# Kernel tuning notes

Measured on AMD Instinct MI355X. Metric: run time of the kernel, lower is better.

## Reference

```python
import jax, jax.numpy as jnp
import numpy as np

B, N, IN_DIM, OUT_DIM, H = 8, 1024, 256, 256, 4
HD = OUT_DIM // H  # head_dim = 64
NEG = -1e9
EPS = 1e-5


def setup_inputs() -> dict:
    key = jax.random.key(0)
    ks = jax.random.split(key, 9)
    h = jax.random.normal(ks[0], (B, N, IN_DIM), dtype=jnp.float32)
    adj = jax.random.randint(ks[1], (N, N), 0, 2, dtype=jnp.int32)
    adj = adj.at[jnp.arange(N), jnp.arange(N)].set(1)  # self loops so no empty rows
    s = 1.0 / np.sqrt(IN_DIM)
    W = jax.random.uniform(ks[2], (H, IN_DIM, HD), jnp.float32, -s, s)
    sa = 1.0 / np.sqrt(2 * HD)
    a1 = jax.random.uniform(ks[3], (H, HD), jnp.float32, -sa, sa)
    a2 = jax.random.uniform(ks[4], (H, HD), jnp.float32, -sa, sa)
    sp = 1.0 / np.sqrt(OUT_DIM)
    proj_w = jax.random.uniform(ks[5], (OUT_DIM, OUT_DIM), jnp.float32, -sp, sp)
    proj_b = jax.random.uniform(ks[6], (OUT_DIM,), jnp.float32, -sp, sp)
    gamma = jnp.ones((OUT_DIM,), jnp.float32)
    beta = jnp.zeros((OUT_DIM,), jnp.float32)
    return {"h": h, "adj": adj, "W": W, "a1": a1, "a2": a2,
            "proj_w": proj_w, "proj_b": proj_b, "gamma": gamma, "beta": beta}


def reference(h, adj, W, a1, a2, proj_w, proj_b, gamma, beta):
    # Wh: [B,H,N,HD]
    Wh = jnp.einsum('bni,hid->bhnd', h, W)
    # Decompose a([Wh_i || Wh_j]) = a1.Wh_i + a2.Wh_j (same math as concat+linear)
    si = jnp.einsum('bhnd,hd->bhn', Wh, a1)  # [B,H,N]
    sj = jnp.einsum('bhnd,hd->bhn', Wh, a2)
    e = jax.nn.leaky_relu(si[:, :, :, None] + sj[:, :, None, :], 0.2)  # [B,H,N,N]
    mask = (adj == 0)  # [N,N]
    e = jnp.where(mask[None, None], NEG, e)
    alpha = jax.nn.softmax(e, axis=-1)
    out = jnp.einsum('bhnm,bhmd->bhnd', alpha, Wh)  # [B,H,N,HD]
    h_multi = out.transpose(0, 2, 1, 3).reshape(B, N, OUT_DIM)  # concat heads
    h_out = jnp.einsum('bnd,od->bno', h_multi, proj_w) + proj_b
    h_out = h_out + h  # residual (in_dim == out_dim)
    mu = jnp.mean(h_out, axis=-1, keepdims=True)
    var = jnp.mean(jnp.square(h_out - mu), axis=-1, keepdims=True)
    return (h_out - mu) * jax.lax.rsqrt(var + EPS) * gamma + beta
```

## Files before the change

kernel.cpp:

```cpp
#include <hip/hip_runtime.h>
#include <hip/hip_bf16.h>

#define NN 1024
#define LOG2E 1.44269504088896f

typedef __attribute__((ext_vector_type(8))) short short8;
typedef __attribute__((ext_vector_type(4))) short short4e;
typedef __attribute__((ext_vector_type(4))) float floatx4;
typedef __attribute__((ext_vector_type(4))) int intx4;
typedef __attribute__((ext_vector_type(2))) int intx2;

static __device__ __forceinline__ unsigned pk2(float f0, float f1) {
    unsigned u0 = __float_as_uint(f0) + 0x8000u;
    unsigned u1 = __float_as_uint(f1) + 0x8000u;
    return __builtin_amdgcn_perm(u1, u0, 0x07060302u);
}
static __device__ __forceinline__ short8 pk8(floatx4 v0, floatx4 v1) {
    union { intx4 i; short8 s; } u;
    u.i[0] = (int)pk2(v0[0], v0[1]); u.i[1] = (int)pk2(v0[2], v0[3]);
    u.i[2] = (int)pk2(v1[0], v1[1]); u.i[3] = (int)pk2(v1[2], v1[3]);
    return u.s;
}

__global__ __launch_bounds__(256) void prep_kernel(
    const float* __restrict__ W, const float* __restrict__ proj_w,
    const int* __restrict__ adj,
    __hip_bfloat16* __restrict__ WTb,
    __hip_bfloat16* __restrict__ pwb,
    unsigned* __restrict__ adjm)
{
    int blk = blockIdx.x, t = threadIdx.x;
    if (blk < 16) {
        int o = blk * 16 + (t >> 4);
        int hh = o >> 6, d = o & 63;
        #pragma unroll
        for (int kk = 0; kk < 16; ++kk) {
            int k = (t & 15) + 16 * kk;
            WTb[(size_t)o * 256 + k] = __float2bfloat16(W[((size_t)hh * 256 + k) * 64 + d]);
        }
    } else if (blk < 32) {
        size_t base = (size_t)(blk - 16) * 4096 + (size_t)t * 16;
        #pragma unroll
        for (int k = 0; k < 16; k += 8) {
            floatx4 v0 = *(const floatx4*)(proj_w + base + k);
            floatx4 v1 = *(const floatx4*)(proj_w + base + k + 4);
            *(short8*)(pwb + base + k) = pk8(v0, v1);
        }
    } else {
        int n = (blk - 32) * 8 + (t >> 5);
        int wd = t & 31;
        const int* arow = adj + (size_t)n * NN + wd * 32;
        unsigned bits = 0;
        #pragma unroll
        for (int j4 = 0; j4 < 8; ++j4) {
            intx4 v = *(const intx4*)(arow + j4 * 4);
            #pragma unroll
            for (int j = 0; j < 4; ++j) if (v[j] != 0) bits |= (1u << (j4 * 4 + j));
        }
        adjm[(size_t)n * 32 + wd] = bits;
    }
}

__global__ __launch_bounds__(256) void wh_kernel(
    const float* __restrict__ h,
    const __hip_bfloat16* __restrict__ WTb,
    const float* __restrict__ a1, const float* __restrict__ a2,
    __hip_bfloat16* __restrict__ WhT,
    float* __restrict__ si, float* __restrict__ sj)
{
    int t = threadIdx.x;
    int w = t >> 6, l = t & 63;
    int rl = l & 15, q = l >> 4;
    int r0 = blockIdx.x * 16;
    int bb = r0 >> 10, n0 = r0 & 1023;

    __shared__ __align__(16) __hip_bfloat16 bst[4][16][264];
    __shared__ float redsi[4][4][16];
    __shared__ float redsj[4][4][16];

    short8 af[8];
    const float* Arow = h + (size_t)(r0 + rl) * 256 + q * 8;
    #pragma unroll
    for (int k0 = 0; k0 < 8; ++k0) {
        floatx4 v0 = *(const floatx4*)(Arow + k0 * 32);
        floatx4 v1 = *(const floatx4*)(Arow + k0 * 32 + 4);
        af[k0] = pk8(v0, v1);
    }

    short8 sreg[8], nreg[8];
    {
        const __hip_bfloat16* src = WTb + (size_t)w * 16 * 256;
        #pragma unroll
        for (int k = 0; k < 8; ++k) sreg[k] = *(const short8*)(src + k * 512 + l * 8);
    }

    #pragma unroll
    for (int j = 0; j < 4; ++j) {
        if (j < 3) {
            const __hip_bfloat16* src = WTb + (size_t)(w + 4 * (j + 1)) * 16 * 256;
            #pragma unroll
            for (int k = 0; k < 8; ++k) nreg[k] = *(const short8*)(src + k * 512 + l * 8);
        }
        #pragma unroll
        for (int k = 0; k < 8; ++k)
            *(short8*)(&bst[w][k * 2 + (l >> 5)][(l & 31) * 8]) = sreg[k];
        floatx4 acc = {0.f, 0.f, 0.f, 0.f};
        #pragma unroll
        for (int k0 = 0; k0 < 8; ++k0) {
            short8 bf = *(const short8*)(&bst[w][rl][q * 8 + k0 * 32]);
            acc = __builtin_amdgcn_mfma_f32_16x16x32_bf16(af[k0], bf, acc, 0, 0, 0);
        }

        intx2 pr;
        pr[0] = (int)pk2(acc[0], acc[1]);
        pr[1] = (int)pk2(acc[2], acc[3]);
        *(intx2*)(WhT + ((size_t)(bb * 4 + j) * 64 + w * 16 + rl) * NN + n0 + q * 4) = pr;

        float av1 = a1[j * 64 + w * 16 + rl] * LOG2E;
        float av2 = a2[j * 64 + w * 16 + rl] * LOG2E;
        #pragma unroll
        for (int i = 0; i < 4; ++i) {
            float p1 = acc[i] * av1, p2 = acc[i] * av2;
            #pragma unroll
            for (int off = 1; off < 16; off <<= 1) {
                p1 += __shfl_xor(p1, off, 64);
                p2 += __shfl_xor(p2, off, 64);
            }
            if (rl == 0) { redsi[w][j][q * 4 + i] = p1; redsj[w][j][q * 4 + i] = p2; }
        }
        #pragma unroll
        for (int z = 0; z < 8; ++z) sreg[z] = nreg[z];
    }
    __syncthreads();

    if (t < 64) {
        int head = t >> 4, row = t & 15;
        si[(size_t)(bb * 4 + head) * NN + n0 + row] =
            redsi[0][head][row] + redsi[1][head][row] + redsi[2][head][row] + redsi[3][head][row];
    } else if (t < 128) {
        int u = t - 64;
        int head = u >> 4, row = u & 15;
        sj[(size_t)(bb * 4 + head) * NN + n0 + row] =
            redsj[0][head][row] + redsj[1][head][row] + redsj[2][head][row] + redsj[3][head][row];
    }
}

__global__ __launch_bounds__(256) void attn_kernel(
    const unsigned* __restrict__ adjm,
    const __hip_bfloat16* __restrict__ WhT,
    const float* __restrict__ si, const float* __restrict__ sj,
    __hip_bfloat16* __restrict__ hmb)
{
    int bx = blockIdx.x, t = threadIdx.x;
    int w = t >> 6, l = t & 63;
    int rl = l & 15, q = l >> 4;
    int b = bx >> 6, n0 = (bx & 63) * 16;
    int bh = b * 4 + w;

    __shared__ __align__(16) __hip_bfloat16 bst[4][64][72];
    __shared__ __align__(16) __hip_bfloat16 p_lds[4][16][72];
    __shared__ float rinvs[4][16];

    int r = l >> 2, cg = l & 3;
    float sii = si[(size_t)bh * NN + n0 + r];
    const float* sjr = sj + (size_t)bh * NN;
    const unsigned* amrow = adjm + (size_t)(n0 + r) * 32;

    float lsum = 0.f;
    floatx4 acc[4] = { {0,0,0,0}, {0,0,0,0}, {0,0,0,0}, {0,0,0,0} };

    const __hip_bfloat16* Bsrc = WhT + (size_t)bh * 64 * NN;

    short8 sreg[8], nreg[8];
    #pragma unroll
    for (int k = 0; k < 8; ++k)
        sreg[k] = *(const short8*)(Bsrc + (size_t)(k * 8 + (l >> 3)) * NN + (l & 7) * 8);

    #pragma unroll
    for (int it = 0; it < 16; ++it) {
        int m0 = it * 64;
        if (it < 15) {
            int m1 = m0 + 64;
            #pragma unroll
            for (int k = 0; k < 8; ++k)
                nreg[k] = *(const short8*)(Bsrc + (size_t)(k * 8 + (l >> 3)) * NN + m1 + (l & 7) * 8);
        }
        {
            int mb = m0 + cg * 16;
            unsigned bits = amrow[(m0 >> 5) + (cg >> 1)] >> ((cg & 1) * 16);
            unsigned pkd[4];
            #pragma unroll
            for (int c4 = 0; c4 < 4; ++c4) {
                floatx4 s4 = *(const floatx4*)(sjr + mb + c4 * 4);
                float pv[4];
                #pragma unroll
                for (int k = 0; k < 4; ++k) {
                    float x = sii + s4[k];
                    x = fmaxf(x, 0.2f * x);
                    x = ((bits >> (c4 * 4 + k)) & 1u) ? x : -1e9f;
                    pv[k] = exp2f(x);
                    lsum += pv[k];
                }
                pkd[c4] = 0;
                pkd[c4] = (unsigned)pk2(pv[0], pv[1]) | 0u;
                unsigned hi = pk2(pv[2], pv[3]);
                intx2 two; two[0] = (int)pkd[c4]; two[1] = (int)hi;
                *(intx2*)(&p_lds[w][r][cg * 16 + c4 * 4]) = two;
            }
        }
        #pragma unroll
        for (int k = 0; k < 8; ++k)
            *(short8*)(&bst[w][k * 8 + (l >> 3)][(l & 7) * 8]) = sreg[k];
        #pragma unroll
        for (int ks = 0; ks < 2; ++ks) {
            short8 afr = *(const short8*)(&p_lds[w][rl][q * 8 + ks * 32]);
            #pragma unroll
            for (int dt = 0; dt < 4; ++dt) {
                short8 bfr = *(const short8*)(&bst[w][dt * 16 + rl][q * 8 + ks * 32]);
                acc[dt] = __builtin_amdgcn_mfma_f32_16x16x32_bf16(afr, bfr, acc[dt], 0, 0, 0);
            }
        }
        #pragma unroll
        for (int z = 0; z < 8; ++z) sreg[z] = nreg[z];
    }

    lsum += __shfl_xor(lsum, 1, 64);
    lsum += __shfl_xor(lsum, 2, 64);
    if (cg == 0) rinvs[w][r] = 1.f / lsum;
    float riv[4];
    #pragma unroll
    for (int i = 0; i < 4; ++i) riv[i] = rinvs[w][q * 4 + i];

    #pragma unroll
    for (int dt = 0; dt < 4; ++dt) {
        #pragma unroll
        for (int i = 0; i < 4; ++i) {
            float v = acc[dt][i] * riv[i];
            unsigned uv = (__float_as_uint(v) + 0x8000u) >> 16;
            hmb[((size_t)(b * NN) + n0 + q * 4 + i) * 256 + w * 64 + dt * 16 + rl] =
                __ushort_as_bfloat16((unsigned short)uv);
        }
    }
}

__global__ __launch_bounds__(256) void proj_ln_kernel(
    const __hip_bfloat16* __restrict__ hmb,
    const float* __restrict__ h,
    const __hip_bfloat16* __restrict__ pwb,
    const float* __restrict__ proj_b, const float* __restrict__ gamma,
    const float* __restrict__ beta,
    float* __restrict__ out)
{
    int t = threadIdx.x;
    int w = t >> 6, l = t & 63;
    int rl = l & 15, q = l >> 4;
    int r0 = blockIdx.x * 16;

    __shared__ __align__(16) __hip_bfloat16 bst[4][16][264];
    __shared__ float red[2][4][16];

    short8 af[8];
    const __hip_bfloat16* Arow = hmb + (size_t)(r0 + rl) * 256 + q * 8;
    #pragma unroll
    for (int k0 = 0; k0 < 8; ++k0) af[k0] = *(const short8*)(Arow + k0 * 32);

    short8 sreg[8], nreg[8];
    {
        const __hip_bfloat16* src = pwb + (size_t)w * 16 * 256;
        #pragma unroll
        for (int k = 0; k < 8; ++k) sreg[k] = *(const short8*)(src + k * 512 + l * 8);
    }

    floatx4 pacc[4];
    #pragma unroll
    for (int j = 0; j < 4; ++j) {
        if (j < 3) {
            const __hip_bfloat16* src = pwb + (size_t)(w + 4 * (j + 1)) * 16 * 256;
            #pragma unroll
            for (int k = 0; k < 8; ++k) nreg[k] = *(const short8*)(src + k * 512 + l * 8);
        }
        #pragma unroll
        for (int k = 0; k < 8; ++k)
            *(short8*)(&bst[w][k * 2 + (l >> 5)][(l & 31) * 8]) = sreg[k];
        floatx4 a = {0.f, 0.f, 0.f, 0.f};
        #pragma unroll
        for (int k0 = 0; k0 < 8; ++k0) {
            short8 bf = *(const short8*)(&bst[w][rl][q * 8 + k0 * 32]);
            a = __builtin_amdgcn_mfma_f32_16x16x32_bf16(af[k0], bf, a, 0, 0, 0);
        }
        pacc[j] = a;
        #pragma unroll
        for (int z = 0; z < 8; ++z) sreg[z] = nreg[z];
    }

    float ps[4] = {0.f, 0.f, 0.f, 0.f};
    #pragma unroll
    for (int j = 0; j < 4; ++j) {
        int col = (w + j * 4) * 16 + rl;
        float pb = proj_b[col];
        #pragma unroll
        for (int i = 0; i < 4; ++i) {
            float v = pacc[j][i] + pb + h[(size_t)(r0 + q * 4 + i) * 256 + col];
            pacc[j][i] = v;
            ps[i] += v;
        }
    }
    #pragma unroll
    for (int i = 0; i < 4; ++i) {
        float s = ps[i];
        #pragma unroll
        for (int off = 1; off < 16; off <<= 1) s += __shfl_xor(s, off, 64);
        ps[i] = s;
    }
    if (rl == 0) {
        for (int i = 0; i < 4; ++i) red[0][w][q * 4 + i] = ps[i];
    }
    __syncthreads();
    float mu[4];
    #pragma unroll
    for (int i = 0; i < 4; ++i) {
        int row = q * 4 + i;
        mu[i] = (red[0][0][row] + red[0][1][row] + red[0][2][row] + red[0][3][row]) * (1.f / 256.f);
    }
    float vs[4] = {0.f, 0.f, 0.f, 0.f};
    #pragma unroll
    for (int j = 0; j < 4; ++j) {
        #pragma unroll
        for (int i = 0; i < 4; ++i) { float cv = pacc[j][i] - mu[i]; vs[i] += cv * cv; }
    }
    #pragma unroll
    for (int i = 0; i < 4; ++i) {
        float s = vs[i];
        #pragma unroll
        for (int off = 1; off < 16; off <<= 1) s += __shfl_xor(s, off, 64);
        vs[i] = s;
    }
    if (rl == 0) {
        for (int i = 0; i < 4; ++i) red[1][w][q * 4 + i] = vs[i];
    }
    __syncthreads();
    float rs[4];
    #pragma unroll
    for (int i = 0; i < 4; ++i) {
        int row = q * 4 + i;
        float var = (red[1][0][row] + red[1][1][row] + red[1][2][row] + red[1][3][row]) * (1.f / 256.f);
        rs[i] = rsqrtf(var + 1e-5f);
    }
    #pragma unroll
    for (int j = 0; j < 4; ++j) {
        int col = (w + j * 4) * 16 + rl;
        float g = gamma[col], be = beta[col];
        #pragma unroll
        for (int i = 0; i < 4; ++i)
            out[(size_t)(r0 + q * 4 + i) * 256 + col] = (pacc[j][i] - mu[i]) * rs[i] * g + be;
    }
}

extern "C" void kernel_launch(void* const* d_in, const int* in_sizes, int n_in,
                              void* d_out, int out_size, void* d_ws, size_t ws_size,
                              hipStream_t stream) {
    const float* h      = (const float*)d_in[0];
    const int*   adj    = (const int*)d_in[1];
    const float* W      = (const float*)d_in[2];
    const float* a1     = (const float*)d_in[3];
    const float* a2     = (const float*)d_in[4];
    const float* proj_w = (const float*)d_in[5];
    const float* proj_b = (const float*)d_in[6];
    const float* gamma  = (const float*)d_in[7];
    const float* beta   = (const float*)d_in[8];
    float* out = (float*)d_out;

    char* ws = (char*)d_ws;
    __hip_bfloat16* WhT = (__hip_bfloat16*)ws;   ws += (size_t)32 * 64 * NN * 2;
    __hip_bfloat16* hmb = (__hip_bfloat16*)ws;   ws += (size_t)8 * NN * 256 * 2;
    __hip_bfloat16* WTb = (__hip_bfloat16*)ws;   ws += 256 * 256 * 2;
    __hip_bfloat16* pwb = (__hip_bfloat16*)ws;   ws += 256 * 256 * 2;
    float* si = (float*)ws;                      ws += (size_t)32 * NN * 4;
    float* sj = (float*)ws;                      ws += (size_t)32 * NN * 4;
    unsigned* adjm = (unsigned*)ws;              ws += (size_t)NN * 32 * 4;

    prep_kernel<<<160, 256, 0, stream>>>(W, proj_w, adj, WTb, pwb, adjm);
    wh_kernel<<<512, 256, 0, stream>>>(h, WTb, a1, a2, WhT, si, sj);
    attn_kernel<<<512, 256, 0, stream>>>(adjm, WhT, si, sj, hmb);
    proj_ln_kernel<<<512, 256, 0, stream>>>(hmb, h, pwb, proj_b, gamma, beta, out);
}
```

Measured before the change: 125.2 us.

## Fuse attention and projection+layernorm kernels via shared-memory handoff

Merges the attention kernel and the projection/LayerNorm kernel into one launch. Each block now writes its 16x256 attention output into LDS instead of global memory and immediately runs the projection, residual and LayerNorm on it. Shared memory is aliased between the two phases. This removes the hmb global round trip and one kernel launch, at the cost of extra barriers and higher register pressure in the fused kernel.

```diff
diff --git a/kernel.cpp b/kernel.cpp
--- a/kernel.cpp
+++ b/kernel.cpp
@@ -145,21 +145,30 @@
     }
 }
 
-__global__ __launch_bounds__(256) void attn_kernel(
+__global__ __launch_bounds__(256) void attn_proj_kernel(
     const unsigned* __restrict__ adjm,
     const __hip_bfloat16* __restrict__ WhT,
     const float* __restrict__ si, const float* __restrict__ sj,
-    __hip_bfloat16* __restrict__ hmb)
+    const __hip_bfloat16* __restrict__ pwb,
+    const float* __restrict__ h,
+    const float* __restrict__ proj_b, const float* __restrict__ gamma,
+    const float* __restrict__ beta,
+    float* __restrict__ out)
 {
+    __shared__ __align__(16) char smem[46592];
+    auto bst   = reinterpret_cast<__hip_bfloat16 (*)[64][72]>(smem);
+    auto pl    = reinterpret_cast<__hip_bfloat16 (*)[16][72]>(smem + 36864);
+    auto rinvs = reinterpret_cast<float (*)[16]>(smem + 46080);
+    auto pbst  = reinterpret_cast<__hip_bfloat16 (*)[16][264]>(smem);
+    auto hm    = reinterpret_cast<__hip_bfloat16 (*)[264]>(smem + 36864);
+    auto red   = reinterpret_cast<float (*)[4][16]>(smem + 45312);
+
     int bx = blockIdx.x, t = threadIdx.x;
     int w = t >> 6, l = t & 63;
     int rl = l & 15, q = l >> 4;
     int b = bx >> 6, n0 = (bx & 63) * 16;
     int bh = b * 4 + w;
-
-    __shared__ __align__(16) __hip_bfloat16 bst[4][64][72];
-    __shared__ __align__(16) __hip_bfloat16 p_lds[4][16][72];
-    __shared__ float rinvs[4][16];
+    int r0 = bx * 16;
 
     int r = l >> 2, cg = l & 3;
     float sii = si[(size_t)bh * NN + n0 + r];
@@ -188,7 +197,6 @@
         {
             int mb = m0 + cg * 16;
             unsigned bits = amrow[(m0 >> 5) + (cg >> 1)] >> ((cg & 1) * 16);
-            unsigned pkd[4];
             #pragma unroll
             for (int c4 = 0; c4 < 4; ++c4) {
                 floatx4 s4 = *(const floatx4*)(sjr + mb + c4 * 4);
@@ -201,11 +209,10 @@
                     pv[k] = exp2f(x);
                     lsum += pv[k];
                 }
-                pkd[c4] = 0;
-                pkd[c4] = (unsigned)pk2(pv[0], pv[1]) | 0u;
-                unsigned hi = pk2(pv[2], pv[3]);
-                intx2 two; two[0] = (int)pkd[c4]; two[1] = (int)hi;
-                *(intx2*)(&p_lds[w][r][cg * 16 + c4 * 4]) = two;
+                intx2 two;
+                two[0] = (int)pk2(pv[0], pv[1]);
+                two[1] = (int)pk2(pv[2], pv[3]);
+                *(intx2*)(&pl[w][r][cg * 16 + c4 * 4]) = two;
             }
         }
         #pragma unroll
@@ -213,7 +220,7 @@
             *(short8*)(&bst[w][k * 8 + (l >> 3)][(l & 7) * 8]) = sreg[k];
         #pragma unroll
         for (int ks = 0; ks < 2; ++ks) {
-            short8 afr = *(const short8*)(&p_lds[w][rl][q * 8 + ks * 32]);
+            short8 afr = *(const short8*)(&pl[w][rl][q * 8 + ks * 32]);
             #pragma unroll
             for (int dt = 0; dt < 4; ++dt) {
                 short8 bfr = *(const short8*)(&bst[w][dt * 16 + rl][q * 8 + ks * 32]);
@@ -231,45 +238,27 @@
     #pragma unroll
     for (int i = 0; i < 4; ++i) riv[i] = rinvs[w][q * 4 + i];
 
-    #pragma unroll
-    for (int dt = 0; dt < 4; ++dt) {
-        #pragma unroll
-        for (int i = 0; i < 4; ++i) {
-            float v = acc[dt][i] * riv[i];
-            unsigned uv = (__float_as_uint(v) + 0x8000u) >> 16;
-            hmb[((size_t)(b * NN) + n0 + q * 4 + i) * 256 + w * 64 + dt * 16 + rl] =
-                __ushort_as_bfloat16((unsigned short)uv);
-        }
-    }
-}
-
-__global__ __launch_bounds__(256) void proj_ln_kernel(
-    const __hip_bfloat16* __restrict__ hmb,
-    const float* __restrict__ h,
-    const __hip_bfloat16* __restrict__ pwb,
-    const float* __restrict__ proj_b, const float* __restrict__ gamma,
-    const float* __restrict__ beta,
-    float* __restrict__ out)
-{
-    int t = threadIdx.x;
-    int w = t >> 6, l = t & 63;
-    int rl = l & 15, q = l >> 4;
-    int r0 = blockIdx.x * 16;
-
-    __shared__ __align__(16) __hip_bfloat16 bst[4][16][264];
-    __shared__ float red[2][4][16];
-
-    short8 af[8];
-    const __hip_bfloat16* Arow = hmb + (size_t)(r0 + rl) * 256 + q * 8;
-    #pragma unroll
-    for (int k0 = 0; k0 < 8; ++k0) af[k0] = *(const short8*)(Arow + k0 * 32);
-
-    short8 sreg[8], nreg[8];
+    short8 psreg[8], pnreg[8];
     {
         const __hip_bfloat16* src = pwb + (size_t)w * 16 * 256;
         #pragma unroll
-        for (int k = 0; k < 8; ++k) sreg[k] = *(const short8*)(src + k * 512 + l * 8);
-    }
+        for (int k = 0; k < 8; ++k) psreg[k] = *(const short8*)(src + k * 512 + l * 8);
+    }
+
+    __syncthreads();
+    #pragma unroll
+    for (int dt = 0; dt < 4; ++dt) {
+        #pragma unroll
+        for (int i = 0; i < 4; ++i) {
+            unsigned uv = (__float_as_uint(acc[dt][i] * riv[i]) + 0x8000u) >> 16;
+            hm[q * 4 + i][w * 64 + dt * 16 + rl] = __ushort_as_bfloat16((unsigned short)uv);
+        }
+    }
+    __syncthreads();
+
+    short8 paf[8];
+    #pragma unroll
+    for (int k0 = 0; k0 < 8; ++k0) paf[k0] = *(const short8*)(&hm[rl][q * 8 + k0 * 32]);
 
     floatx4 pacc[4];
     #pragma unroll
@@ -277,20 +266,20 @@
         if (j < 3) {
             const __hip_bfloat16* src = pwb + (size_t)(w + 4 * (j + 1)) * 16 * 256;
             #pragma unroll
-            for (int k = 0; k < 8; ++k) nreg[k] = *(const short8*)(src + k * 512 + l * 8);
+            for (int k = 0; k < 8; ++k) pnreg[k] = *(const short8*)(src + k * 512 + l * 8);
         }
         #pragma unroll
         for (int k = 0; k < 8; ++k)
-            *(short8*)(&bst[w][k * 2 + (l >> 5)][(l & 31) * 8]) = sreg[k];
+            *(short8*)(&pbst[w][k * 2 + (l >> 5)][(l & 31) * 8]) = psreg[k];
         floatx4 a = {0.f, 0.f, 0.f, 0.f};
         #pragma unroll
         for (int k0 = 0; k0 < 8; ++k0) {
-            short8 bf = *(const short8*)(&bst[w][rl][q * 8 + k0 * 32]);
-            a = __builtin_amdgcn_mfma_f32_16x16x32_bf16(af[k0], bf, a, 0, 0, 0);
+            short8 bf = *(const short8*)(&pbst[w][rl][q * 8 + k0 * 32]);
+            a = __builtin_amdgcn_mfma_f32_16x16x32_bf16(paf[k0], bf, a, 0, 0, 0);
         }
         pacc[j] = a;
         #pragma unroll
-        for (int z = 0; z < 8; ++z) sreg[z] = nreg[z];
+        for (int z = 0; z < 8; ++z) psreg[z] = pnreg[z];
     }
 
     float ps[4] = {0.f, 0.f, 0.f, 0.f};
@@ -372,7 +361,6 @@
 
     char* ws = (char*)d_ws;
     __hip_bfloat16* WhT = (__hip_bfloat16*)ws;   ws += (size_t)32 * 64 * NN * 2;
-    __hip_bfloat16* hmb = (__hip_bfloat16*)ws;   ws += (size_t)8 * NN * 256 * 2;
     __hip_bfloat16* WTb = (__hip_bfloat16*)ws;   ws += 256 * 256 * 2;
     __hip_bfloat16* pwb = (__hip_bfloat16*)ws;   ws += 256 * 256 * 2;
     float* si = (float*)ws;                      ws += (size_t)32 * NN * 4;
@@ -381,6 +369,5 @@
 
     prep_kernel<<<160, 256, 0, stream>>>(W, proj_w, adj, WTb, pwb, adjm);
     wh_kernel<<<512, 256, 0, stream>>>(h, WTb, a1, a2, WhT, si, sj);
-    attn_kernel<<<512, 256, 0, stream>>>(adjm, WhT, si, sj, hmb);
-    proj_ln_kernel<<<512, 256, 0, stream>>>(hmb, h, pwb, proj_b, gamma, beta, out);
-}
+    attn_proj_kernel<<<512, 256, 0, stream>>>(adjm, WhT, si, sj, pwb, h, proj_b, gamma, beta, out);
+}
```

Result: faster. 122.1 us (-2.5%).
